# Kernel tuning notes

Hardware: AMD Instinct MI355X
Metric: run time of the kernel (lower is better)

## Reference

```python
import jax, jax.numpy as jnp
import numpy as np
from jax import lax

K = 2000      # node_num of GraphConvolution
H, W = 75, 100  # edge_region_feature spatial grid (from per-pixel concat loops)


def setup_inputs() -> dict:
    key = jax.random.key(0)
    k1, k2, k3, k4 = jax.random.split(key, 4)
    b, c = 8, 512
    edge_region_feature = jax.random.normal(k1, (b, c, H, W), dtype=jnp.float32)
    edge_region_predict = jax.random.normal(k2, (b, 3, H, W), dtype=jnp.float32)
    # GraphConvolution params: kaiming_normal_(fan_out) weights, zero bias
    w1 = jax.random.normal(k3, (512, 128), dtype=jnp.float32) * np.sqrt(2.0 / 128)
    b1 = jnp.zeros((K, 128), dtype=jnp.float32)
    w2 = jax.random.normal(k4, (128, 128), dtype=jnp.float32) * np.sqrt(2.0 / 128)
    b2 = jnp.zeros((K, 128), dtype=jnp.float32)
    return {"edge_region_feature": edge_region_feature,
            "edge_region_predict": edge_region_predict,
            "w1": w1, "b1": b1, "w2": w2, "b2": b2}


def reference(edge_region_feature, edge_region_predict, w1, b1, w2, b2):
    b, c = edge_region_feature.shape[0], edge_region_feature.shape[1]
    # block_feature built as: for x in range(W) for y in range(H) -> node n at (y=n%H, x=n//H)
    block = jnp.transpose(edge_region_feature, (0, 3, 2, 1)).reshape(b, W * H, c)  # (b, 7500, 512)

    # topk over channel-0 prediction, flattened row-major (idx = y*W + x)
    scores = edge_region_predict[:, 0, :, :].reshape(b, -1)            # (b, 7500)
    _vals, topk_idx = lax.top_k(scores, K)
    sorted_idx = jnp.sort(topk_idx, axis=1)                            # (b, 2000) int32

    # gather node features (replicates original's indexing of block_feature)
    node_map = jnp.take_along_axis(block, sorted_idx[:, :, None], axis=1)  # (b, 2000, 512)

    # generate_adjacent_map: decode positions with width=W, connect 8-neighborhood (+self)
    py = sorted_idx // W
    px = sorted_idx % W
    near_y = jnp.abs(py[:, :, None] - py[:, None, :]) <= 1
    near_x = jnp.abs(px[:, :, None] - px[:, None, :]) <= 1
    adj = (near_y & near_x).astype(jnp.float32)                        # (b, 2000, 2000)

    # node_feature_grouping = ReLU6 -> GCN(512->128) -> GCN(128->128)
    inp = jnp.clip(jnp.concatenate([adj, node_map], axis=2), 0.0, 6.0)  # ReLU6 on cat(adj, nodes)
    a = inp[:, :, :K]
    nf = inp[:, :, K:]
    # GCN1: A @ X @ W1 + b1  (in!=out -> no residual)
    x1 = jnp.einsum('bij,bjf->bif', a, nf) @ w1 + b1                   # (b, 2000, 128)
    # GCN2: A @ X1 @ W2 + b2 + X1 (in==out -> residual)
    x2 = jnp.einsum('bij,bjf->bif', a, x1) @ w2 + b2 + x1              # (b, 2000, 128)

    node_output_feature = jnp.tanh(x2)
    return node_output_feature, sorted_idx
```

## Files before the change

kernel.cpp:

```cpp
#include <hip/hip_runtime.h>
#include <cmath>

#define H_DIM 75
#define W_DIM 100
#define HW 7500
#define KSEL 2000
#define BATCH 8
#define CIN 512
#define FDIM 128

typedef short v4s __attribute__((ext_vector_type(4)));
typedef short v8s __attribute__((ext_vector_type(8)));
typedef float v16f __attribute__((ext_vector_type(16)));

__device__ __forceinline__ unsigned int map_key(float f) {
  unsigned int u = __float_as_uint(f);
  return (u & 0x80000000u) ? ~u : (u | 0x80000000u);
}

__device__ __forceinline__ float fast_tanh(float x) {
  float e = __expf(2.0f * x);
  return 1.0f - 2.0f * __builtin_amdgcn_rcpf(e + 1.0f);
}

__device__ __forceinline__ unsigned short bf16_rne(float v) {
  unsigned int u = __float_as_uint(v);
  unsigned int r = u + 0x7FFFu + ((u >> 16) & 1u);
  return (unsigned short)(r >> 16);
}
__device__ __forceinline__ float bf16_to_f(unsigned short h) {
  return __uint_as_float(((unsigned int)h) << 16);
}

__global__ __launch_bounds__(1024) void topk_nbr_kernel(
    const float* __restrict__ pred, const float* __restrict__ w1,
    const float* __restrict__ w2,
    int* __restrict__ off2_ws, int* __restrict__ perm_ws,
    float* __restrict__ out_idx,
    unsigned short* __restrict__ nbr, unsigned char* __restrict__ cnt,
    unsigned short* __restrict__ w1t_hi, unsigned short* __restrict__ w1t_lo,
    unsigned short* __restrict__ w2t_hi, unsigned short* __restrict__ w2t_lo)
{
  __shared__ unsigned int keys[HW];
  __shared__ unsigned int whist[16 * 256];
  __shared__ unsigned int hist[256];
  __shared__ unsigned int partials[16];
  __shared__ unsigned int s_prefix, s_kth;
  const int tid = threadIdx.x;

  if (blockIdx.x >= BATCH) {
    int base = (blockIdx.x - BATCH) * 1024 + tid;
    for (int e = base; e < CIN * FDIM + FDIM * FDIM; e += 8 * 1024) {
      if (e < CIN * FDIM) {
        int k = e & (CIN - 1), f = e >> 9;
        float v = w1[k * FDIM + f];
        unsigned short hi = bf16_rne(v);
        unsigned short lo = bf16_rne(v - bf16_to_f(hi));
        w1t_hi[(size_t)f * CIN + k] = hi;
        w1t_lo[(size_t)f * CIN + k] = lo;
      } else {
        int e2 = e - CIN * FDIM;
        int k = e2 & (FDIM - 1), f = e2 >> 7;
        float v = w2[k * FDIM + f];
        unsigned short hi = bf16_rne(v);
        unsigned short lo = bf16_rne(v - bf16_to_f(hi));
        w2t_hi[(size_t)f * FDIM + k] = hi;
        w2t_lo[(size_t)f * FDIM + k] = lo;
      }
    }
    return;
  }

  const int b = blockIdx.x;
  const int lane = tid & 63, w = tid >> 6;
  const float* scores = pred + (size_t)b * 3 * HW;
  for (int i = tid; i < HW; i += 1024) keys[i] = map_key(scores[i]);
  if (tid == 0) { s_prefix = 0u; s_kth = KSEL; }
  __syncthreads();

  for (int shift = 24; shift >= 0; shift -= 8) {
    for (int i = tid; i < 16 * 256; i += 1024) whist[i] = 0u;
    __syncthreads();
    unsigned int pref = s_prefix;
    unsigned int maskhi = (shift == 24) ? 0u : (0xFFFFFFFFu << (shift + 8));
    for (int i = tid; i < HW; i += 1024) {
      unsigned int k = keys[i];
      if ((k & maskhi) == pref)
        atomicAdd(&whist[w * 256 + ((k >> shift) & 0xFFu)], 1u);
    }
    __syncthreads();
    if (tid < 256) {
      unsigned int s = 0;
      #pragma unroll
      for (int ww = 0; ww < 16; ++ww) s += whist[ww * 256 + tid];
      hist[tid] = s;
    }
    __syncthreads();
    if (tid < 64) {
      unsigned int b0 = hist[tid * 4], b1 = hist[tid * 4 + 1];
      unsigned int b2 = hist[tid * 4 + 2], b3 = hist[tid * 4 + 3];
      unsigned int kth = s_kth;
      unsigned int T = b0 + b1 + b2 + b3;
      #pragma unroll
      for (int off = 1; off < 64; off <<= 1) {
        unsigned int t = __shfl_down(T, off, 64);
        if (tid + off < 64) T += t;
      }
      unsigned int U = __shfl_down(T, 1, 64);
      if (tid == 63) U = 0u;
      unsigned int s3 = b3 + U, s2 = b2 + s3, s1 = b1 + s2, s0 = b0 + s1;
      if (s0 >= kth && s1 < kth) { s_prefix = pref | ((unsigned)(4 * tid + 0) << shift); s_kth = kth - s1; }
      if (s1 >= kth && s2 < kth) { s_prefix = pref | ((unsigned)(4 * tid + 1) << shift); s_kth = kth - s2; }
      if (s2 >= kth && s3 < kth) { s_prefix = pref | ((unsigned)(4 * tid + 2) << shift); s_kth = kth - s3; }
      if (s3 >= kth && U  < kth) { s_prefix = pref | ((unsigned)(4 * tid + 3) << shift); s_kth = kth - U; }
    }
    __syncthreads();
  }
  const unsigned int thresh = s_prefix;

  unsigned int local[8];
  unsigned int sum = 0;
  #pragma unroll
  for (int e = 0; e < 8; ++e) {
    int i = tid * 8 + e;
    unsigned int p = 0;
    if (i < HW) {
      unsigned int ky = keys[i];
      if (ky > thresh) p = 1u;
      else if (ky == thresh) p = (1u << 16);
    }
    local[e] = p; sum += p;
  }
  __syncthreads();
  short* pos_of  = (short*)keys;
  int*   s_idx_sh = (int*)((char*)keys + 15000);
  for (int i = tid; i < HW; i += 1024) pos_of[i] = -1;

  unsigned int inc = sum;
  #pragma unroll
  for (int off = 1; off < 64; off <<= 1) {
    unsigned int t = __shfl_up(inc, off, 64);
    if (lane >= off) inc += t;
  }
  if (lane == 63) partials[w] = inc;
  __syncthreads();
  if (tid < 16) {
    unsigned int v = partials[tid];
    #pragma unroll
    for (int off = 1; off < 16; off <<= 1) {
      unsigned int t = __shfl_up(v, off, 64);
      if (tid >= off) v += t;
    }
    partials[tid] = v;
  }
  __syncthreads();
  unsigned int total = partials[15];
  unsigned int run = (w ? partials[w - 1] : 0u) + inc - sum;
  unsigned int ties = (unsigned int)KSEL - (total & 0xFFFFu);
  #pragma unroll
  for (int e = 0; e < 8; ++e) {
    int i = tid * 8 + e;
    unsigned int p = local[e];
    unsigned int gt_pref = run & 0xFFFFu;
    unsigned int eq_pref = run >> 16;
    bool sel = (p & 1u) || (((p >> 16) != 0u) && eq_pref < ties);
    if (sel) {
      unsigned int pos = gt_pref + (eq_pref < ties ? eq_pref : ties);
      out_idx[b * KSEL + pos] = (float)i;
      s_idx_sh[pos] = i;
      pos_of[i] = (short)pos;
    }
    run += p;
  }
  __syncthreads();

  if (tid < 128) hist[tid] = 0u;
  __syncthreads();
  for (int pos = tid; pos < KSEL; pos += 1024)
    atomicAdd(&hist[s_idx_sh[pos] % H_DIM], 1u);
  __syncthreads();
  if (tid == 0) {
    unsigned int run2 = 0u;
    for (int j = 0; j < H_DIM; ++j) { unsigned int t = hist[j]; hist[j] = run2; run2 += t; }
  }
  __syncthreads();
  for (int pos = tid; pos < KSEL; pos += 1024) {
    int i = s_idx_sh[pos];
    int y = i % H_DIM;
    unsigned int j = atomicAdd(&hist[y], 1u);
    off2_ws[b * KSEL + j] = (i % H_DIM) * W_DIM + i / H_DIM;
    perm_ws[b * KSEL + j] = pos;
  }

  for (int i = tid; i < KSEL; i += 1024) {
    int q = s_idx_sh[i];
    int py = q / W_DIM, px = q % W_DIM;
    unsigned short tmp[9];
    int c = 0;
    #pragma unroll
    for (int dy = -1; dy <= 1; ++dy) {
      int y = py + dy;
      if ((unsigned)y >= (unsigned)H_DIM) continue;
      #pragma unroll
      for (int dx = -1; dx <= 1; ++dx) {
        int x = px + dx;
        if ((unsigned)x >= (unsigned)W_DIM) continue;
        short p = pos_of[y * W_DIM + x];
        if (p >= 0) tmp[c++] = (unsigned short)p;
      }
    }
    #pragma unroll
    for (int t = 0; t < 9; ++t)
      nbr[(size_t)(b * KSEL + i) * 9 + t] = (t < c) ? tmp[t] : (unsigned short)0;
    cnt[b * KSEL + i] = (unsigned char)c;
  }
}

__global__ __launch_bounds__(256) void gemm1_fused(
    const float* __restrict__ feat, const int* __restrict__ off2_ws,
    const int* __restrict__ perm_ws,
    const unsigned short* __restrict__ w1t_hi,
    const unsigned short* __restrict__ w1t_lo,
    float* __restrict__ G)
{
  __shared__ unsigned short a_hi[2][64][20], a_lo[2][64][20];
  const int b = blockIdx.y;
  const int n0 = blockIdx.x * 64;
  const int tid = threadIdx.x;
  const int lane = tid & 63, w = tid >> 6;
  const int wr = w & 1, wc = w >> 1;
  const int q = lane >> 5, m = lane & 31;
  v16f acc0, acc1;
  #pragma unroll
  for (int i = 0; i < 16; ++i) { acc0[i] = 0.f; acc1[i] = 0.f; }
  const int an = wr * 32 + m;
  const int f0 = wc * 64 + m;
  const int n_st = tid & 63, ks = (tid >> 6) * 4;
  int nidx = n0 + n_st;
  if (nidx > KSEL - 1) nidx = KSEL - 1;
  const float* fb = feat + (size_t)b * CIN * HW + off2_ws[b * KSEL + nidx];

  #pragma unroll
  for (int j = 0; j < 4; ++j) {
    float v = fb[(size_t)(ks + j) * HW];
    v = fminf(fmaxf(v, 0.f), 6.f);
    unsigned short hi = bf16_rne(v);
    a_hi[0][n_st][ks + j] = hi;
    a_lo[0][n_st][ks + j] = bf16_rne(v - bf16_to_f(hi));
  }
  __syncthreads();

  for (int kk = 0; kk < CIN; kk += 16) {
    const int p = (kk >> 4) & 1;
    if (kk + 16 < CIN) {
      #pragma unroll
      for (int j = 0; j < 4; ++j) {
        float v = fb[(size_t)(kk + 16 + ks + j) * HW];
        v = fminf(fmaxf(v, 0.f), 6.f);
        unsigned short hi = bf16_rne(v);
        a_hi[p ^ 1][n_st][ks + j] = hi;
        a_lo[p ^ 1][n_st][ks + j] = bf16_rne(v - bf16_to_f(hi));
      }
    }
    v4s ah0 = *(const v4s*)&a_hi[p][an][q * 8];
    v4s ah1 = *(const v4s*)&a_hi[p][an][q * 8 + 4];
    v4s al0 = *(const v4s*)&a_lo[p][an][q * 8];
    v4s al1 = *(const v4s*)&a_lo[p][an][q * 8 + 4];
    v8s avh = __builtin_shufflevector(ah0, ah1, 0, 1, 2, 3, 4, 5, 6, 7);
    v8s avl = __builtin_shufflevector(al0, al1, 0, 1, 2, 3, 4, 5, 6, 7);
    v8s b0h = *(const v8s*)&w1t_hi[(size_t)f0 * CIN + kk + q * 8];
    v8s b0l = *(const v8s*)&w1t_lo[(size_t)f0 * CIN + kk + q * 8];
    v8s b1h = *(const v8s*)&w1t_hi[(size_t)(f0 + 32) * CIN + kk + q * 8];
    v8s b1l = *(const v8s*)&w1t_lo[(size_t)(f0 + 32) * CIN + kk + q * 8];
    acc0 = __builtin_amdgcn_mfma_f32_32x32x16_bf16(avh, b0h, acc0, 0, 0, 0);
    acc0 = __builtin_amdgcn_mfma_f32_32x32x16_bf16(avh, b0l, acc0, 0, 0, 0);
    acc0 = __builtin_amdgcn_mfma_f32_32x32x16_bf16(avl, b0h, acc0, 0, 0, 0);
    acc1 = __builtin_amdgcn_mfma_f32_32x32x16_bf16(avh, b1h, acc1, 0, 0, 0);
    acc1 = __builtin_amdgcn_mfma_f32_32x32x16_bf16(avh, b1l, acc1, 0, 0, 0);
    acc1 = __builtin_amdgcn_mfma_f32_32x32x16_bf16(avl, b1h, acc1, 0, 0, 0);
    __syncthreads();
  }
  float* ob = G + (size_t)b * KSEL * FDIM;
  const int* pb = perm_ws + b * KSEL;
  #pragma unroll
  for (int reg = 0; reg < 16; ++reg) {
    int row = n0 + wr * 32 + (reg & 3) + 8 * (reg >> 2) + 4 * q;
    if (row < KSEL) {
      int pr = pb[row];
      ob[(size_t)pr * FDIM + f0]      = acc0[reg];
      ob[(size_t)pr * FDIM + f0 + 32] = acc1[reg];
    }
  }
}

__global__ __launch_bounds__(512) void gemm2_fused(
    const float* __restrict__ G, const float* __restrict__ b1,
    const unsigned short* __restrict__ nbr, const unsigned char* __restrict__ cnt,
    const unsigned short* __restrict__ w2t_hi,
    const unsigned short* __restrict__ w2t_lo,
    float* __restrict__ x1, float* __restrict__ Hm)
{
  __shared__ __align__(16) unsigned short xh[64][FDIM];
  __shared__ __align__(16) unsigned short xl[64][FDIM];
  const int b = blockIdx.y;
  const int n0 = blockIdx.x * 64;
  const int tid = threadIdx.x;
  const int g = tid >> 5, lane32 = tid & 31;
  const float4* G4 = (const float4*)G + (size_t)b * KSEL * 32;

  #pragma unroll
  for (int rr = 0; rr < 4; ++rr) {
    const int r = rr * 16 + g;
    const int node = n0 + r;
    const int nodec = (node > KSEL - 1) ? KSEL - 1 : node;
    const size_t bi = (size_t)b * KSEL + nodec;
    const unsigned short* nb = nbr + bi * 9;
    unsigned short idx[9];
    #pragma unroll
    for (int t = 0; t < 9; ++t) idx[t] = nb[t];
    const int c = cnt[bi];
    float4 v[9];
    #pragma unroll
    for (int t = 0; t < 9; ++t) v[t] = G4[(size_t)idx[t] * 32 + lane32];
    float4 acc = ((const float4*)b1)[nodec * 32 + lane32];
    #pragma unroll
    for (int t = 0; t < 9; ++t) {
      float mk = (t < c) ? 1.f : 0.f;
      acc.x = fmaf(v[t].x, mk, acc.x);
      acc.y = fmaf(v[t].y, mk, acc.y);
      acc.z = fmaf(v[t].z, mk, acc.z);
      acc.w = fmaf(v[t].w, mk, acc.w);
    }
    if (node < KSEL) ((float4*)x1)[bi * 32 + lane32] = acc;
    ushort4 h, l;
    h.x = bf16_rne(acc.x); l.x = bf16_rne(acc.x - bf16_to_f(h.x));
    h.y = bf16_rne(acc.y); l.y = bf16_rne(acc.y - bf16_to_f(h.y));
    h.z = bf16_rne(acc.z); l.z = bf16_rne(acc.z - bf16_to_f(h.z));
    h.w = bf16_rne(acc.w); l.w = bf16_rne(acc.w - bf16_to_f(h.w));
    const int cs = (lane32 * 4) ^ ((r & 15) << 3);
    *(ushort4*)&xh[r][cs] = h;
    *(ushort4*)&xl[r][cs] = l;
  }
  __syncthreads();

  if (tid < 256) {
    const int lane = tid & 63, w = tid >> 6;
    const int wr = w & 1, wc = w >> 1;
    const int q = lane >> 5, m = lane & 31;
    const int ar = wr * 32 + m;
    const int f0 = wc * 64 + m;
    v16f acc0, acc1;
    #pragma unroll
    for (int i = 0; i < 16; ++i) { acc0[i] = 0.f; acc1[i] = 0.f; }
    #pragma unroll
    for (int k0 = 0; k0 < FDIM; k0 += 16) {
      const int ac = (k0 + q * 8) ^ ((ar & 15) << 3);
      v8s avh = *(const v8s*)&xh[ar][ac];
      v8s avl = *(const v8s*)&xl[ar][ac];
      v8s b0h = *(const v8s*)&w2t_hi[(size_t)f0 * FDIM + k0 + q * 8];
      v8s b0l = *(const v8s*)&w2t_lo[(size_t)f0 * FDIM + k0 + q * 8];
      v8s b1h = *(const v8s*)&w2t_hi[(size_t)(f0 + 32) * FDIM + k0 + q * 8];
      v8s b1l = *(const v8s*)&w2t_lo[(size_t)(f0 + 32) * FDIM + k0 + q * 8];
      acc0 = __builtin_amdgcn_mfma_f32_32x32x16_bf16(avh, b0h, acc0, 0, 0, 0);
      acc0 = __builtin_amdgcn_mfma_f32_32x32x16_bf16(avh, b0l, acc0, 0, 0, 0);
      acc0 = __builtin_amdgcn_mfma_f32_32x32x16_bf16(avl, b0h, acc0, 0, 0, 0);
      acc1 = __builtin_amdgcn_mfma_f32_32x32x16_bf16(avh, b1h, acc1, 0, 0, 0);
      acc1 = __builtin_amdgcn_mfma_f32_32x32x16_bf16(avh, b1l, acc1, 0, 0, 0);
      acc1 = __builtin_amdgcn_mfma_f32_32x32x16_bf16(avl, b1h, acc1, 0, 0, 0);
    }
    float* ob = Hm + (size_t)b * KSEL * FDIM;
    #pragma unroll
    for (int reg = 0; reg < 16; ++reg) {
      int row = n0 + wr * 32 + (reg & 3) + 8 * (reg >> 2) + 4 * q;
      if (row < KSEL) {
        ob[(size_t)row * FDIM + f0]      = acc0[reg];
        ob[(size_t)row * FDIM + f0 + 32] = acc1[reg];
      }
    }
  }
}

__global__ __launch_bounds__(512) void out_kernel(
    const float* __restrict__ Hm, const float* __restrict__ x1,
    const float* __restrict__ b2,
    const unsigned short* __restrict__ nbr, const unsigned char* __restrict__ cnt,
    float* __restrict__ out)
{
  const int g = threadIdx.x >> 5, lane = threadIdx.x & 31;
  const int node = blockIdx.x * 16 + g;
  const int bb = blockIdx.y;
  const size_t bi = (size_t)bb * KSEL + node;
  const unsigned short* nb = nbr + bi * 9;
  unsigned short idx[9];
  #pragma unroll
  for (int t = 0; t < 9; ++t) idx[t] = nb[t];
  const int c = cnt[bi];
  const float4* H4 = (const float4*)Hm + (size_t)bb * KSEL * 32;
  float4 v[9];
  #pragma unroll
  for (int t = 0; t < 9; ++t) v[t] = H4[(size_t)idx[t] * 32 + lane];
  float4 acc = ((const float4*)b2)[node * 32 + lane];
  float4 xv = ((const float4*)x1)[bi * 32 + lane];
  acc.x += xv.x; acc.y += xv.y; acc.z += xv.z; acc.w += xv.w;
  #pragma unroll
  for (int t = 0; t < 9; ++t) {
    float mk = (t < c) ? 1.f : 0.f;
    acc.x = fmaf(v[t].x, mk, acc.x);
    acc.y = fmaf(v[t].y, mk, acc.y);
    acc.z = fmaf(v[t].z, mk, acc.z);
    acc.w = fmaf(v[t].w, mk, acc.w);
  }
  float4 r;
  r.x = fast_tanh(acc.x); r.y = fast_tanh(acc.y);
  r.z = fast_tanh(acc.z); r.w = fast_tanh(acc.w);
  ((float4*)out)[bi * 32 + lane] = r;
}

extern "C" void kernel_launch(void* const* d_in, const int* in_sizes, int n_in,
                              void* d_out, int out_size, void* d_ws, size_t ws_size,
                              hipStream_t stream) {
  const float* feat = (const float*)d_in[0];
  const float* pred = (const float*)d_in[1];
  const float* w1   = (const float*)d_in[2];
  const float* b1   = (const float*)d_in[3];
  const float* w2   = (const float*)d_in[4];
  const float* b2   = (const float*)d_in[5];
  float* out0 = (float*)d_out;
  float* out_idx = out0 + (size_t)BATCH * KSEL * FDIM;

  char* ws = (char*)d_ws;
  int*            off2_ws = (int*)(ws + 0);
  int*            perm_ws = (int*)(ws + 64256);
  unsigned short* nbr     = (unsigned short*)(ws + 128512);
  unsigned char*  cnt     = (unsigned char*)(ws + 416512);
  float*          G       = (float*)(ws + 432640);
  float*          x1      = (float*)(ws + 8624640);
  float*          Hm      = (float*)(ws + 16816640);
  unsigned short* w1t_hi  = (unsigned short*)(ws + 25008640);
  unsigned short* w1t_lo  = (unsigned short*)(ws + 25139712);
  unsigned short* w2t_hi  = (unsigned short*)(ws + 25270784);
  unsigned short* w2t_lo  = (unsigned short*)(ws + 25303552);

  topk_nbr_kernel<<<BATCH + 8, 1024, 0, stream>>>(
      pred, w1, w2, off2_ws, perm_ws, out_idx, nbr, cnt,
      w1t_hi, w1t_lo, w2t_hi, w2t_lo);
  gemm1_fused<<<dim3(32, BATCH), 256, 0, stream>>>(
      feat, off2_ws, perm_ws, w1t_hi, w1t_lo, G);
  gemm2_fused<<<dim3(32, BATCH), 512, 0, stream>>>(G, b1, nbr, cnt, w2t_hi, w2t_lo, x1, Hm);
  out_kernel<<<dim3(KSEL / 16, BATCH), 512, 0, stream>>>(Hm, x1, b2, nbr, cnt, out0);
}
```

Before: 232.0 us.

## Compute feature projection densely over all pixels instead of gathered top-k nodes

Replaces the gathered GEMM1 (only the 2000 selected nodes, with gather offsets and a permuted scatter) with a dense GEMM over all 7500 spatial positions, writing G in spatial order into a padded buffer. Neighbour lists now hold both the spatial index, used by gemm2 to gather G rows, and the sorted position, used by the output kernel. This removes the histogram/permutation stage from the topk kernel and makes feature reads contiguous. It also lets gemm1 no longer depend on the top-k result. The cost is about 3.75x more GEMM1 compute and a much larger intermediate buffer.

```diff
diff --git a/kernel.cpp b/kernel.cpp
--- a/kernel.cpp
+++ b/kernel.cpp
@@ -4,6 +4,7 @@
 #define H_DIM 75
 #define W_DIM 100
 #define HW 7500
+#define HWPAD 7552
 #define KSEL 2000
 #define BATCH 8
 #define CIN 512
@@ -35,9 +36,9 @@
 __global__ __launch_bounds__(1024) void topk_nbr_kernel(
     const float* __restrict__ pred, const float* __restrict__ w1,
     const float* __restrict__ w2,
-    int* __restrict__ off2_ws, int* __restrict__ perm_ws,
     float* __restrict__ out_idx,
-    unsigned short* __restrict__ nbr, unsigned char* __restrict__ cnt,
+    unsigned short* __restrict__ nbr_sp, unsigned short* __restrict__ nbr_pos,
+    unsigned char* __restrict__ cnt,
     unsigned short* __restrict__ w1t_hi, unsigned short* __restrict__ w1t_lo,
     unsigned short* __restrict__ w2t_hi, unsigned short* __restrict__ w2t_lo)
 {
@@ -174,28 +175,10 @@
   }
   __syncthreads();
 
-  if (tid < 128) hist[tid] = 0u;
-  __syncthreads();
-  for (int pos = tid; pos < KSEL; pos += 1024)
-    atomicAdd(&hist[s_idx_sh[pos] % H_DIM], 1u);
-  __syncthreads();
-  if (tid == 0) {
-    unsigned int run2 = 0u;
-    for (int j = 0; j < H_DIM; ++j) { unsigned int t = hist[j]; hist[j] = run2; run2 += t; }
-  }
-  __syncthreads();
-  for (int pos = tid; pos < KSEL; pos += 1024) {
-    int i = s_idx_sh[pos];
-    int y = i % H_DIM;
-    unsigned int j = atomicAdd(&hist[y], 1u);
-    off2_ws[b * KSEL + j] = (i % H_DIM) * W_DIM + i / H_DIM;
-    perm_ws[b * KSEL + j] = pos;
-  }
-
   for (int i = tid; i < KSEL; i += 1024) {
     int q = s_idx_sh[i];
     int py = q / W_DIM, px = q % W_DIM;
-    unsigned short tmp[9];
+    unsigned short tsp[9], tpo[9];
     int c = 0;
     #pragma unroll
     for (int dy = -1; dy <= 1; ++dy) {
@@ -205,20 +188,26 @@
       for (int dx = -1; dx <= 1; ++dx) {
         int x = px + dx;
         if ((unsigned)x >= (unsigned)W_DIM) continue;
-        short p = pos_of[y * W_DIM + x];
-        if (p >= 0) tmp[c++] = (unsigned short)p;
+        int j = y * W_DIM + x;
+        short p = pos_of[j];
+        if (p >= 0) {
+          tsp[c] = (unsigned short)((j % H_DIM) * W_DIM + j / H_DIM);
+          tpo[c] = (unsigned short)p;
+          ++c;
+        }
       }
     }
     #pragma unroll
-    for (int t = 0; t < 9; ++t)
-      nbr[(size_t)(b * KSEL + i) * 9 + t] = (t < c) ? tmp[t] : (unsigned short)0;
+    for (int t = 0; t < 9; ++t) {
+      nbr_sp [(size_t)(b * KSEL + i) * 9 + t] = (t < c) ? tsp[t] : (unsigned short)0;
+      nbr_pos[(size_t)(b * KSEL + i) * 9 + t] = (t < c) ? tpo[t] : (unsigned short)0;
+    }
     cnt[b * KSEL + i] = (unsigned char)c;
   }
 }
 
-__global__ __launch_bounds__(256) void gemm1_fused(
-    const float* __restrict__ feat, const int* __restrict__ off2_ws,
-    const int* __restrict__ perm_ws,
+__global__ __launch_bounds__(256) void gemm1_dense(
+    const float* __restrict__ feat,
     const unsigned short* __restrict__ w1t_hi,
     const unsigned short* __restrict__ w1t_lo,
     float* __restrict__ G)
@@ -236,9 +225,9 @@
   const int an = wr * 32 + m;
   const int f0 = wc * 64 + m;
   const int n_st = tid & 63, ks = (tid >> 6) * 4;
-  int nidx = n0 + n_st;
-  if (nidx > KSEL - 1) nidx = KSEL - 1;
-  const float* fb = feat + (size_t)b * CIN * HW + off2_ws[b * KSEL + nidx];
+  int pos = n0 + n_st;
+  if (pos > HW - 1) pos = HW - 1;
+  const float* fb = feat + (size_t)b * CIN * HW + pos;
 
   #pragma unroll
   for (int j = 0; j < 4; ++j) {
@@ -280,22 +269,18 @@
     acc1 = __builtin_amdgcn_mfma_f32_32x32x16_bf16(avl, b1h, acc1, 0, 0, 0);
     __syncthreads();
   }
-  float* ob = G + (size_t)b * KSEL * FDIM;
-  const int* pb = perm_ws + b * KSEL;
+  float* ob = G + (size_t)b * HWPAD * FDIM;
   #pragma unroll
   for (int reg = 0; reg < 16; ++reg) {
     int row = n0 + wr * 32 + (reg & 3) + 8 * (reg >> 2) + 4 * q;
-    if (row < KSEL) {
-      int pr = pb[row];
-      ob[(size_t)pr * FDIM + f0]      = acc0[reg];
-      ob[(size_t)pr * FDIM + f0 + 32] = acc1[reg];
-    }
+    ob[(size_t)row * FDIM + f0]      = acc0[reg];
+    ob[(size_t)row * FDIM + f0 + 32] = acc1[reg];
   }
 }
 
 __global__ __launch_bounds__(512) void gemm2_fused(
     const float* __restrict__ G, const float* __restrict__ b1,
-    const unsigned short* __restrict__ nbr, const unsigned char* __restrict__ cnt,
+    const unsigned short* __restrict__ nbr_sp, const unsigned char* __restrict__ cnt,
     const unsigned short* __restrict__ w2t_hi,
     const unsigned short* __restrict__ w2t_lo,
     float* __restrict__ x1, float* __restrict__ Hm)
@@ -306,7 +291,7 @@
   const int n0 = blockIdx.x * 64;
   const int tid = threadIdx.x;
   const int g = tid >> 5, lane32 = tid & 31;
-  const float4* G4 = (const float4*)G + (size_t)b * KSEL * 32;
+  const float4* G4 = (const float4*)G + (size_t)b * HWPAD * 32;
 
   #pragma unroll
   for (int rr = 0; rr < 4; ++rr) {
@@ -314,7 +299,7 @@
     const int node = n0 + r;
     const int nodec = (node > KSEL - 1) ? KSEL - 1 : node;
     const size_t bi = (size_t)b * KSEL + nodec;
-    const unsigned short* nb = nbr + bi * 9;
+    const unsigned short* nb = nbr_sp + bi * 9;
     unsigned short idx[9];
     #pragma unroll
     for (int t = 0; t < 9; ++t) idx[t] = nb[t];
@@ -383,14 +368,14 @@
 __global__ __launch_bounds__(512) void out_kernel(
     const float* __restrict__ Hm, const float* __restrict__ x1,
     const float* __restrict__ b2,
-    const unsigned short* __restrict__ nbr, const unsigned char* __restrict__ cnt,
+    const unsigned short* __restrict__ nbr_pos, const unsigned char* __restrict__ cnt,
     float* __restrict__ out)
 {
   const int g = threadIdx.x >> 5, lane = threadIdx.x & 31;
   const int node = blockIdx.x * 16 + g;
   const int bb = blockIdx.y;
   const size_t bi = (size_t)bb * KSEL + node;
-  const unsigned short* nb = nbr + bi * 9;
+  const unsigned short* nb = nbr_pos + bi * 9;
   unsigned short idx[9];
   #pragma unroll
   for (int t = 0; t < 9; ++t) idx[t] = nb[t];
@@ -429,23 +414,24 @@
   float* out_idx = out0 + (size_t)BATCH * KSEL * FDIM;
 
   char* ws = (char*)d_ws;
-  int*            off2_ws = (int*)(ws + 0);
-  int*            perm_ws = (int*)(ws + 64256);
-  unsigned short* nbr     = (unsigned short*)(ws + 128512);
-  unsigned char*  cnt     = (unsigned char*)(ws + 416512);
-  float*          G       = (float*)(ws + 432640);
-  float*          x1      = (float*)(ws + 8624640);
-  float*          Hm      = (float*)(ws + 16816640);
-  unsigned short* w1t_hi  = (unsigned short*)(ws + 25008640);
-  unsigned short* w1t_lo  = (unsigned short*)(ws + 25139712);
-  unsigned short* w2t_hi  = (unsigned short*)(ws + 25270784);
-  unsigned short* w2t_lo  = (unsigned short*)(ws + 25303552);
+  unsigned short* nbr_sp  = (unsigned short*)(ws + 0);
+  unsigned short* nbr_pos = (unsigned short*)(ws + 288256);
+  unsigned char*  cnt     = (unsigned char*)(ws + 576512);
+  float*          G       = (float*)(ws + 592640);
+  float*          x1      = (float*)(ws + 31525888);
+  float*          Hm      = (float*)(ws + 39717888);
+  unsigned short* w1t_hi  = (unsigned short*)(ws + 47909888);
+  unsigned short* w1t_lo  = (unsigned short*)(ws + 48040960);
+  unsigned short* w2t_hi  = (unsigned short*)(ws + 48172032);
+  unsigned short* w2t_lo  = (unsigned short*)(ws + 48204800);
 
   topk_nbr_kernel<<<BATCH + 8, 1024, 0, stream>>>(
-      pred, w1, w2, off2_ws, perm_ws, out_idx, nbr, cnt,
+      pred, w1, w2, out_idx, nbr_sp, nbr_pos, cnt,
       w1t_hi, w1t_lo, w2t_hi, w2t_lo);
-  gemm1_fused<<<dim3(32, BATCH), 256, 0, stream>>>(
-      feat, off2_ws, perm_ws, w1t_hi, w1t_lo, G);
-  gemm2_fused<<<dim3(32, BATCH), 512, 0, stream>>>(G, b1, nbr, cnt, w2t_hi, w2t_lo, x1, Hm);
-  out_kernel<<<dim3(KSEL / 16, BATCH), 512, 0, stream>>>(Hm, x1, b2, nbr, cnt, out0);
-}
+  gemm1_dense<<<dim3(HWPAD / 64, BATCH), 256, 0, stream>>>(
+      feat, w1t_hi, w1t_lo, G);
+  gemm2_fused<<<dim3(32, BATCH), 512, 0, stream>>>(
+      G, b1, nbr_sp, cnt, w2t_hi, w2t_lo, x1, Hm);
+  out_kernel<<<dim3(KSEL / 16, BATCH), 512, 0, stream>>>(
+      Hm, x1, b2, nbr_pos, cnt, out0);
+}
```

New measurement: 300.0 us. +29.3%, slower.
